# Kernel optimization log

Hardware: AMD Instinct MI355X
Metric: run time of the kernel (lower is better)

Reference implementation:

```python
import jax, jax.numpy as jnp
import numpy as np

ALPHA = 0.5  # self.alpha


def gcn_conv(x, ei, W, b, n_nodes):
    """PyG GCNConv: sym-normalized A+I aggregation of x @ W.T, plus bias."""
    h = x @ W.T  # [N, H]
    sl = jnp.arange(n_nodes)
    row = jnp.concatenate([ei[0], sl])  # sources (+ self loops)
    col = jnp.concatenate([ei[1], sl])  # targets (+ self loops)
    deg = jax.ops.segment_sum(jnp.ones_like(row, dtype=h.dtype), col, num_segments=n_nodes)
    dinv = jnp.where(deg > 0, jax.lax.rsqrt(deg), 0.0)
    norm = dinv[row] * dinv[col]
    msg = norm[:, None] * h[row]
    out = jax.ops.segment_sum(msg, col, num_segments=n_nodes)
    return out + b


def attention(Ws, A, bA):
    """Bilinear cross-view attention over weight matrices Ws [V, K, D].
    attn[i,j] = sum_k (Ws[i,k] @ A @ Ws[j,k] + bias); row-softmax."""
    K = Ws.shape[1]
    T = jnp.einsum('vka,ab->vkb', Ws, A)
    M = jnp.einsum('vkb,wkb->vw', T, Ws) + K * bA[0]
    return jax.nn.softmax(M, axis=1)


def cross_rep(x_inner, x_lin, att, alpha):
    # temp_i = alpha * sum_j att[i,j] * x_lin[j]; res = (1-alpha) + x_inner + elu(temp)
    cross = alpha * jnp.einsum('vw,wnh->vnh', att, x_lin)
    return (1.0 - alpha) + x_inner + jax.nn.elu(cross)


def setup_inputs() -> dict:
    key = jax.random.key(0)
    ks = jax.random.split(key, 20)
    N, D, H, V, E, Eev = 50000, 128, 128, 3, 800000, 100000
    s_d = 1.0 / np.sqrt(D)
    s_h = 1.0 / np.sqrt(H)
    s_c = 1.0 / np.sqrt(V * H)
    inp = {
        'x': jax.random.normal(ks[0], (N, D), dtype=jnp.float32),
        'W1': jax.random.normal(ks[1], (V, H, D), dtype=jnp.float32) * s_d,
        'b1': jnp.zeros((V, H), dtype=jnp.float32),
        'W2': jax.random.normal(ks[2], (V, H, H), dtype=jnp.float32) * s_h,
        'b2': jnp.zeros((V, H), dtype=jnp.float32),
        'A1': jax.random.normal(ks[3], (D, D), dtype=jnp.float32) * s_d,
        'bA1': jnp.zeros((1,), dtype=jnp.float32),
        'A2': jax.random.normal(ks[4], (H, H), dtype=jnp.float32) * s_h,
        'bA2': jnp.zeros((1,), dtype=jnp.float32),
        'Wc1': jax.random.normal(ks[5], (H, V * H), dtype=jnp.float32) * s_c,
        'bc1': jnp.zeros((H,), dtype=jnp.float32),
        'Wc2': jax.random.normal(ks[6], (H, V * H), dtype=jnp.float32) * s_c,
        'bc2': jnp.zeros((H,), dtype=jnp.float32),
        'edge_index': jax.random.randint(ks[7], (V, 2, E), 0, N, dtype=jnp.int64),
        'edges': jax.random.randint(ks[8], (V, Eev, 2), 0, N, dtype=jnp.int64),
        'edges_neg': jax.random.randint(ks[9], (V, Eev, 2), 0, N, dtype=jnp.int64),
    }
    return inp


def reference(x, W1, b1, W2, b2, A1, bA1, A2, bA2, Wc1, bc1, Wc2, bc2,
              edge_index, edges, edges_neg):
    N = x.shape[0]
    V = W1.shape[0]

    # layer 1: per-view GCNConv + ELU (dropout = identity in eval)
    x1 = jnp.stack([jax.nn.elu(gcn_conv(x, edge_index[v], W1[v], b1[v], N))
                    for v in range(V)])  # [V, N, H]
    xlin1 = jnp.einsum('nd,vhd->vnh', x, W1)  # conv.lin(x) per view
    att1 = attention(W1, A1, bA1)
    xr1 = cross_rep(x1, xlin1, att1, ALPHA)

    # combine 1: concat views along feature dim, linear + ELU
    emb = xr1.transpose(1, 0, 2).reshape(N, -1)  # [N, V*H]
    xc = jax.nn.elu(emb @ Wc1.T + bc1)  # [N, H]

    # layer 2: per-view GCNConv (no activation before cross rep)
    x2 = jnp.stack([gcn_conv(xc, edge_index[v], W2[v], b2[v], N)
                    for v in range(V)])
    xlin2 = jnp.einsum('nd,vhd->vnh', xc, W2)
    att2 = attention(W2, A2, bA2)
    xr2 = cross_rep(x2, xlin2, att2, ALPHA)

    # per-view edge scoring: dot products on pos then neg edges, concatenated
    def score(xv, e_pos, e_neg):
        p = jnp.sum(xv[e_pos[:, 0]] * xv[e_pos[:, 1]], axis=-1)
        n = jnp.sum(xv[e_neg[:, 0]] * xv[e_neg[:, 1]], axis=-1)
        return jnp.concatenate([p, n])

    results = jax.vmap(score)(xr2, edges, edges_neg)  # [V, 2*Eev]
    return results
```

## Files before the change

kernel.cpp:

```cpp
#include <hip/hip_runtime.h>
#include <hip/hip_bf16.h>


#define THREADS 256
#define BCH 8192

typedef __bf16 bf16x8 __attribute__((ext_vector_type(8)));
typedef float f32x4 __attribute__((ext_vector_type(4)));
typedef unsigned short us8 __attribute__((ext_vector_type(8)));

__device__ __forceinline__ float eluf(float x) {
    return x > 0.f ? x : expm1f(x);
}

__device__ __forceinline__ unsigned short f2bf(float f) {
    unsigned u = __builtin_bit_cast(unsigned, f);
    u += 0x7FFF + ((u >> 16) & 1);
    return (unsigned short)(u >> 16);
}
__device__ __forceinline__ float bf2f(unsigned short s) {
    unsigned u = ((unsigned)s) << 16;
    return __builtin_bit_cast(float, u);
}

__global__ __launch_bounds__(THREADS) void init_int_kernel(int* p, int n) {
    int i = blockIdx.x * THREADS + threadIdx.x;
    if (i < n) p[i] = 0;
}


__global__ __launch_bounds__(THREADS) void bucket_count_kernel(
    const int* __restrict__ ei, int* __restrict__ bcnt, int N, int E, int VE) {
    __shared__ int h[160];
    for (int i = threadIdx.x; i < 160; i += THREADS) h[i] = 0;
    __syncthreads();
    int base = blockIdx.x * BCH;
    for (int k = 0; k < BCH; k += THREADS) {
        int t = base + k + threadIdx.x;
        if (t < VE) {
            int v = (t >= E) + (t >= 2 * E);
            int e = t - v * E;
            int col = ei[(size_t)v * 2 * E + E + e];
            atomicAdd(&h[(v * N + col) >> 10], 1);
        }
    }
    __syncthreads();
    for (int i = threadIdx.x; i < 160; i += THREADS)
        if (h[i]) atomicAdd(&bcnt[i], h[i]);
}

__global__ __launch_bounds__(THREADS) void bucket_scan_kernel(
    const int* __restrict__ bcnt, int* __restrict__ bstart, int* __restrict__ bofs, int nb) {
    __shared__ int sh[THREADS];
    int t = threadIdx.x;
    int v = (t < nb) ? bcnt[t] : 0;
    sh[t] = v;
    __syncthreads();
    for (int off = 1; off < THREADS; off <<= 1) {
        int u = (t >= off) ? sh[t - off] : 0;
        __syncthreads();
        sh[t] += u;
        __syncthreads();
    }
    int excl = sh[t] - v;
    if (t < nb) { bstart[t] = excl; bofs[t] = excl; }
    if (t == nb - 1) bstart[nb] = sh[t];
}

__global__ __launch_bounds__(THREADS) void bucket_scatter_kernel(
    const int* __restrict__ ei, int* __restrict__ bofs,
    int* __restrict__ coo_g, int* __restrict__ coo_r, int N, int E, int VE) {
    __shared__ int h[160];
    __shared__ int cur[160];
    for (int i = threadIdx.x; i < 160; i += THREADS) h[i] = 0;
    __syncthreads();
    int base = blockIdx.x * BCH;
    for (int k = 0; k < BCH; k += THREADS) {
        int t = base + k + threadIdx.x;
        if (t < VE) {
            int v = (t >= E) + (t >= 2 * E);
            int e = t - v * E;
            int col = ei[(size_t)v * 2 * E + E + e];
            atomicAdd(&h[(v * N + col) >> 10], 1);
        }
    }
    __syncthreads();
    if (threadIdx.x < 160 && h[threadIdx.x])
        cur[threadIdx.x] = atomicAdd(&bofs[threadIdx.x], h[threadIdx.x]);
    __syncthreads();
    for (int k = 0; k < BCH; k += THREADS) {
        int t = base + k + threadIdx.x;
        if (t < VE) {
            int v = (t >= E) + (t >= 2 * E);
            int e = t - v * E;
            const int* eiv = ei + (size_t)v * 2 * E;
            int row = eiv[e], col = eiv[E + e];
            int g = v * N + col;
            int pos = atomicAdd(&cur[g >> 10], 1);
            coo_g[pos] = g;
            coo_r[pos] = row;
        }
    }
}

__global__ __launch_bounds__(THREADS) void bucket_hist_kernel(
    const int* __restrict__ coo_g, const int* __restrict__ bstart,
    int* __restrict__ cnt, int VN) {
    __shared__ int h[1024];
    for (int i = threadIdx.x; i < 1024; i += THREADS) h[i] = 0;
    __syncthreads();
    int b = blockIdx.x;
    int s = bstart[b], e = bstart[b + 1];
    for (int i = s + threadIdx.x; i < e; i += THREADS)
        atomicAdd(&h[coo_g[i] & 1023], 1);
    __syncthreads();
    int g0 = b << 10;
    for (int i = threadIdx.x; i < 1024; i += THREADS)
        if (g0 + i < VN) cnt[g0 + i] = h[i];
}

__global__ __launch_bounds__(THREADS) void bucket_fill_kernel(
    const int* __restrict__ coo_g, const int* __restrict__ coo_r,
    const int* __restrict__ bstart, int* __restrict__ ptr,
    int* __restrict__ idx, int VN) {
    __shared__ int p[1024];
    int b = blockIdx.x, g0 = b << 10;
    for (int i = threadIdx.x; i < 1024; i += THREADS)
        p[i] = (g0 + i < VN) ? ptr[g0 + i] : 0;
    __syncthreads();
    int s = bstart[b], e = bstart[b + 1];
    for (int i = s + threadIdx.x; i < e; i += THREADS) {
        int pos = atomicAdd(&p[coo_g[i] & 1023], 1);
        idx[pos] = coo_r[i];
    }
    __syncthreads();
    for (int i = threadIdx.x; i < 1024; i += THREADS)
        if (g0 + i < VN) ptr[g0 + i] = p[i];
}

#define SC_T 256
#define SC_CHUNK 1024

__global__ __launch_bounds__(SC_T) void scan_sum_kernel(
    const int* __restrict__ cnt, int* __restrict__ bsum, int n) {
    __shared__ int red[SC_T];
    int base = blockIdx.x * SC_CHUNK + threadIdx.x * 4;
    int s = 0;
#pragma unroll
    for (int k = 0; k < 4; k++) {
        int i = base + k;
        if (i < n) s += cnt[i];
    }
    red[threadIdx.x] = s;
    __syncthreads();
    for (int st = SC_T / 2; st; st >>= 1) {
        if (threadIdx.x < st) red[threadIdx.x] += red[threadIdx.x + st];
        __syncthreads();
    }
    if (threadIdx.x == 0) bsum[blockIdx.x] = red[0];
}

__global__ __launch_bounds__(SC_T) void scan_top_kernel(int* bsum, int nb) {
    __shared__ int sh[SC_T];
    int t = threadIdx.x;
    int v = (t < nb) ? bsum[t] : 0;
    sh[t] = v;
    __syncthreads();
    for (int off = 1; off < SC_T; off <<= 1) {
        int u = (t >= off) ? sh[t - off] : 0;
        __syncthreads();
        sh[t] += u;
        __syncthreads();
    }
    if (t < nb) bsum[t] = sh[t] - v;
}

__global__ __launch_bounds__(SC_T) void scan_apply_kernel(
    const int* __restrict__ cnt, const int* __restrict__ bsum,
    int* __restrict__ ptr, float* __restrict__ dinv, int n) {
    __shared__ int sh[SC_T];
    int base = blockIdx.x * SC_CHUNK + threadIdx.x * 4;
    int v[4];
    int s = 0;
#pragma unroll
    for (int k = 0; k < 4; k++) {
        int i = base + k;
        v[k] = (i < n) ? cnt[i] : 0;
        s += v[k];
    }
    int tin = s;
    sh[threadIdx.x] = s;
    __syncthreads();
    for (int off = 1; off < SC_T; off <<= 1) {
        int u = (threadIdx.x >= off) ? sh[threadIdx.x - off] : 0;
        __syncthreads();
        sh[threadIdx.x] += u;
        __syncthreads();
    }
    int run = bsum[blockIdx.x] + sh[threadIdx.x] - tin;
#pragma unroll
    for (int k = 0; k < 4; k++) {
        int i = base + k;
        if (i < n) {
            ptr[i] = run;
            run += v[k];
            dinv[i] = rsqrtf((float)(v[k] + 1));
        }
    }
}

template <int ABF>
__global__ __launch_bounds__(256) void gemm_bf16_kernel(
    const float* __restrict__ Af, const unsigned short* __restrict__ Ab,
    const float* __restrict__ B, const float* __restrict__ bias,
    unsigned short* __restrict__ C, const float* __restrict__ dscale,
    int M, int Kb, size_t AV, size_t Bz, size_t Cz) {
    __shared__ unsigned short Ah[128 * 64];
    __shared__ unsigned short Bh[128 * 64];
    int tid = threadIdx.x;
    int z = blockIdx.z;
    int m0 = blockIdx.x * 128;
    const float* Bp = B + (size_t)z * Bz;
    int lane = tid & 63, wid = tid >> 6;
    int wr = wid >> 1, wc = wid & 1;
    int lr = lane & 15, lg = lane >> 4;
    f32x4 acc[4][4] = {};

    for (int k0 = 0; k0 < Kb; k0 += 64) {
        size_t Abase = (size_t)(k0 >> 7) * AV + (k0 & 127);
        for (int i = 0; i < 4; ++i) {
            int ch = tid + i * 256;
            int row = ch >> 3, c8 = (ch & 7) << 3;
            int e = (row * 64 + c8) ^ ((row & 7) << 3);
            int gm = m0 + row;
            us8 h8;
            if (ABF) {
                if (gm < M) {
                    h8 = *(const us8*)(Ab + Abase + (size_t)gm * 128 + c8);
                } else {
#pragma unroll
                    for (int j = 0; j < 8; j++) h8[j] = 0;
                }
            } else {
                float va[8];
                if (gm < M) {
                    const float* p = Af + Abase + (size_t)gm * 128 + c8;
                    *(float4*)(va)     = *(const float4*)(p);
                    *(float4*)(va + 4) = *(const float4*)(p + 4);
                } else {
#pragma unroll
                    for (int j = 0; j < 8; j++) va[j] = 0.f;
                }
#pragma unroll
                for (int j = 0; j < 8; j++) h8[j] = f2bf(va[j]);
            }
            *(us8*)&Ah[e] = h8;
            float vb[8];
            const float* q = Bp + (size_t)row * Kb + k0 + c8;
            *(float4*)(vb)     = *(const float4*)(q);
            *(float4*)(vb + 4) = *(const float4*)(q + 4);
            us8 b8;
#pragma unroll
            for (int j = 0; j < 8; j++) b8[j] = f2bf(vb[j]);
            *(us8*)&Bh[e] = b8;
        }
        __syncthreads();
#pragma unroll
        for (int ks = 0; ks < 2; ++ks) {
            bf16x8 ah[4], bh[4];
#pragma unroll
            for (int m = 0; m < 4; m++) {
                int row = wr * 64 + m * 16 + lr;
                int e = (row * 64 + ks * 32 + lg * 8) ^ ((row & 7) << 3);
                ah[m] = *(const bf16x8*)&Ah[e];
            }
#pragma unroll
            for (int n = 0; n < 4; n++) {
                int col = wc * 64 + n * 16 + lr;
                int e = (col * 64 + ks * 32 + lg * 8) ^ ((col & 7) << 3);
                bh[n] = *(const bf16x8*)&Bh[e];
            }
#pragma unroll
            for (int m = 0; m < 4; m++)
#pragma unroll
                for (int n = 0; n < 4; n++)
                    acc[m][n] = __builtin_amdgcn_mfma_f32_16x16x32_bf16(ah[m], bh[n], acc[m][n], 0, 0, 0);
        }
        __syncthreads();
    }

#pragma unroll
    for (int m = 0; m < 4; m++) {
        int rbase = m0 + wr * 64 + m * 16 + lg * 4;
#pragma unroll
        for (int n = 0; n < 4; n++) {
            int col = wc * 64 + n * 16 + lr;
#pragma unroll
            for (int j = 0; j < 4; j++) {
                int row = rbase + j;
                if (row < M) {
                    float vv = acc[m][n][j];
                    if (bias) vv = eluf(vv + bias[col]);
                    if (dscale) vv *= dscale[(size_t)z * M + row];
                    C[(size_t)z * Cz + (size_t)row * 128 + col] = f2bf(vv);
                }
            }
        }
    }
}

__global__ __launch_bounds__(THREADS) void small_mm_nn_kernel(
    const float* __restrict__ W1, const float* __restrict__ W2,
    const float* __restrict__ A1, const float* __restrict__ A2,
    float* __restrict__ T) {
    int lin = blockIdx.x * THREADS + threadIdx.x;
    if (lin >= 2 * 3 * 128 * 128) return;
    int l = lin / 49152;
    int rem = lin - l * 49152;
    int b = rem & 127;
    int vk = rem >> 7;
    const float* w = (l ? W2 : W1) + (size_t)vk * 128;
    const float* A = l ? A2 : A1;
    float s = 0.f;
#pragma unroll 8
    for (int a = 0; a < 128; a++) s += w[a] * A[a * 128 + b];
    T[lin] = s;
}

__global__ __launch_bounds__(THREADS) void att_reduce_kernel(
    const float* __restrict__ T, const float* __restrict__ W1,
    const float* __restrict__ W2, const float* __restrict__ bA1,
    const float* __restrict__ bA2, float* __restrict__ Mraw) {
    int l = blockIdx.x / 9;
    int vw = blockIdx.x - l * 9;
    int v = vw / 3, w = vw - v * 3;
    const float* tp = T + (size_t)l * 49152 + (size_t)v * 16384;
    const float* wp = (l ? W2 : W1) + (size_t)w * 16384;
    float s = 0.f;
    for (int i = threadIdx.x; i < 16384; i += THREADS) s += tp[i] * wp[i];
    __shared__ float red[THREADS];
    red[threadIdx.x] = s;
    __syncthreads();
    for (int st = THREADS / 2; st; st >>= 1) {
        if (threadIdx.x < st) red[threadIdx.x] += red[threadIdx.x + st];
        __syncthreads();
    }
    if (threadIdx.x == 0) Mraw[blockIdx.x] = red[0] + 128.f * (l ? bA2[0] : bA1[0]);
}

__global__ void att_softmax_kernel(const float* __restrict__ Mraw, float* __restrict__ att) {
    int v = threadIdx.x;
    if (v >= 6) return;
    float m0 = Mraw[v * 3 + 0], m1 = Mraw[v * 3 + 1], m2 = Mraw[v * 3 + 2];
    float mx = fmaxf(m0, fmaxf(m1, m2));
    float e0 = expf(m0 - mx), e1 = expf(m1 - mx), e2 = expf(m2 - mx);
    float s = e0 + e1 + e2;
    att[v * 3 + 0] = e0 / s;
    att[v * 3 + 1] = e1 / s;
    att[v * 3 + 2] = e2 / s;
}

__global__ __launch_bounds__(THREADS) void gather_cross_kernel(
    const unsigned short* __restrict__ xs, const float* __restrict__ dinv,
    const int* __restrict__ ptr, const int* __restrict__ idx,
    const float* __restrict__ att, const float* __restrict__ bias,
    unsigned short* __restrict__ xr, int N, int elu_inner) {
    int wv = (blockIdx.x * THREADS + threadIdx.x) >> 6;
    int lane = threadIdx.x & 63;
    int VN = 3 * N;
    if (wv >= VN) return;
    int v = wv / N;
    int n = wv - v * N;
    int vN = v * N;
    int g = lane >> 4, f0 = (lane & 15) * 8;

    float acc[8] = {};
    int s = (wv == 0) ? 0 : ptr[wv - 1];
    int e = ptr[wv];
    int j = s + g;
    for (; j + 12 < e; j += 16) {
        int r0 = idx[j], r1 = idx[j + 4], r2 = idx[j + 8], r3 = idx[j + 12];
        us8 u0 = *(const us8*)(xs + (((size_t)(vN + r0)) << 7) + f0);
        us8 u1 = *(const us8*)(xs + (((size_t)(vN + r1)) << 7) + f0);
        us8 u2 = *(const us8*)(xs + (((size_t)(vN + r2)) << 7) + f0);
        us8 u3 = *(const us8*)(xs + (((size_t)(vN + r3)) << 7) + f0);
#pragma unroll
        for (int i = 0; i < 8; i++)
            acc[i] += (bf2f(u0[i]) + bf2f(u1[i])) + (bf2f(u2[i]) + bf2f(u3[i]));
    }
    for (; j < e; j += 4) {
        int r0 = idx[j];
        us8 u0 = *(const us8*)(xs + (((size_t)(vN + r0)) << 7) + f0);
#pragma unroll
        for (int i = 0; i < 8; i++) acc[i] += bf2f(u0[i]);
    }
#pragma unroll
    for (int i = 0; i < 8; i++) {
        acc[i] += __shfl_xor(acc[i], 16);
        acc[i] += __shfl_xor(acc[i], 32);
    }

    if (g == 0) {
        us8 su = *(const us8*)(xs + (((size_t)wv) << 7) + f0);
        float dc = dinv[wv];
        size_t nb = (((size_t)n) << 7) + f0;
        size_t NH = ((size_t)N) << 7;
        us8 c0 = *(const us8*)(xs + nb);
        us8 c1 = *(const us8*)(xs + NH + nb);
        us8 c2 = *(const us8*)(xs + 2 * NH + nb);
        float wa = att[v * 3 + 0] / dinv[n];
        float wb = att[v * 3 + 1] / dinv[N + n];
        float wc = att[v * 3 + 2] / dinv[2 * N + n];
        float4 bb0 = *(const float4*)(bias + v * 128 + f0);
        float4 bb1 = *(const float4*)(bias + v * 128 + f0 + 4);
        float bv[8] = {bb0.x, bb0.y, bb0.z, bb0.w, bb1.x, bb1.y, bb1.z, bb1.w};
        us8 o;
#pragma unroll
        for (int i = 0; i < 8; i++) {
            float a = dc * (acc[i] + bf2f(su[i])) + bv[i];
            if (elu_inner) a = eluf(a);
            float cr = wa * bf2f(c0[i]) + wb * bf2f(c1[i]) + wc * bf2f(c2[i]);
            o[i] = f2bf(0.5f + a + eluf(0.5f * cr));
        }
        *(us8*)(xr + (((size_t)wv) << 7) + f0) = o;
    }
}

__global__ __launch_bounds__(THREADS) void edge_score_kernel(
    const unsigned short* __restrict__ xr2, const int* __restrict__ edges,
    const int* __restrict__ edges_neg, float* __restrict__ out, int N, int Eev, int V) {
    int q = (blockIdx.x * THREADS + threadIdx.x) >> 4;
    int l16 = threadIdx.x & 15;
    int total = V * 2 * Eev;
    if (q >= total) return;
    int v = q / (2 * Eev);
    int r = q - v * (2 * Eev);
    const int* ep = (r < Eev) ? edges + ((size_t)v * Eev + r) * 2
                              : edges_neg + ((size_t)v * Eev + (r - Eev)) * 2;
    int a = ep[0], b = ep[1];
    const unsigned short* pa = xr2 + (((size_t)v * N + a) << 7) + l16 * 8;
    const unsigned short* pb = xr2 + (((size_t)v * N + b) << 7) + l16 * 8;
    us8 ua = *(const us8*)pa, ub = *(const us8*)pb;
    float s = 0.f;
#pragma unroll
    for (int i = 0; i < 8; i++) s += bf2f(ua[i]) * bf2f(ub[i]);
    s += __shfl_xor(s, 8);
    s += __shfl_xor(s, 4);
    s += __shfl_xor(s, 2);
    s += __shfl_xor(s, 1);
    if (l16 == 0) out[q] = s;
}

extern "C" void kernel_launch(void* const* d_in, const int* in_sizes, int n_in,
                              void* d_out, int out_size, void* d_ws, size_t ws_size,
                              hipStream_t stream) {
    const float* x   = (const float*)d_in[0];
    const float* W1  = (const float*)d_in[1];
    const float* b1  = (const float*)d_in[2];
    const float* W2  = (const float*)d_in[3];
    const float* b2  = (const float*)d_in[4];
    const float* A1  = (const float*)d_in[5];
    const float* bA1 = (const float*)d_in[6];
    const float* A2  = (const float*)d_in[7];
    const float* bA2 = (const float*)d_in[8];
    const float* Wc1 = (const float*)d_in[9];
    const float* bc1 = (const float*)d_in[10];
    const int* ei        = (const int*)d_in[13];
    const int* edges     = (const int*)d_in[14];
    const int* edges_neg = (const int*)d_in[15];
    float* out = (float*)d_out;

    const int H = 128, V = 3;
    const int N = in_sizes[0] / H;
    const int E = in_sizes[13] / (V * 2);
    const int Eev = in_sizes[14] / (V * 2);
    const int VNH = V * N * H;
    const int VN = V * N;
    const int VE = V * E;
    const int NB = (VN + 1023) >> 10;

    float* ws   = (float*)d_ws;
    float* dinv = ws;
    float* T    = dinv + VN;
    float* Mraw = T + 98304;
    float* att  = Mraw + 32;
    int* cnt    = (int*)(att + 32);
    int* ptr    = cnt + VN;
    int* bsum   = ptr + VN;
    int* bcnt   = bsum + 256;
    int* bstart = bcnt + 256;
    int* bofs   = bstart + 256;
    int* idx    = bofs + 256;
    int* coo_g  = idx + VE;
    int* coo_r  = coo_g + VE;
    unsigned short* xs = (unsigned short*)(coo_r + VE);
    unsigned short* xr = xs + VNH;
    unsigned short* xc = xr + VNH;
    (void)ws_size; (void)n_in; (void)out_size;

    dim3 blk(THREADS);
    int gBC = (VE + BCH - 1) / BCH;
    int gGather = (int)(((size_t)VN * 64 + THREADS - 1) / THREADS);
    int nScanB = (VN + SC_CHUNK - 1) / SC_CHUNK;
    dim3 gemmGrid((N + 127) / 128, 1, V);
    dim3 gemmGrid1((N + 127) / 128, 1, 1);
    int gScore = (int)(((size_t)V * 2 * Eev * 16 + THREADS - 1) / THREADS);

    init_int_kernel<<<1, blk, 0, stream>>>(bcnt, 256);
    bucket_count_kernel<<<gBC, blk, 0, stream>>>(ei, bcnt, N, E, VE);
    bucket_scan_kernel<<<1, blk, 0, stream>>>(bcnt, bstart, bofs, NB);
    bucket_scatter_kernel<<<gBC, blk, 0, stream>>>(ei, bofs, coo_g, coo_r, N, E, VE);
    bucket_hist_kernel<<<NB, blk, 0, stream>>>(coo_g, bstart, cnt, VN);
    scan_sum_kernel<<<nScanB, SC_T, 0, stream>>>(cnt, bsum, VN);
    scan_top_kernel<<<1, SC_T, 0, stream>>>(bsum, nScanB);
    scan_apply_kernel<<<nScanB, SC_T, 0, stream>>>(cnt, bsum, ptr, dinv, VN);
    bucket_fill_kernel<<<NB, blk, 0, stream>>>(coo_g, coo_r, bstart, ptr, idx, VN);

    small_mm_nn_kernel<<<(2 * 49152 + THREADS - 1) / THREADS, blk, 0, stream>>>(W1, W2, A1, A2, T);
    att_reduce_kernel<<<18, blk, 0, stream>>>(T, W1, W2, bA1, bA2, Mraw);
    att_softmax_kernel<<<1, 64, 0, stream>>>(Mraw, att);

    gemm_bf16_kernel<0><<<gemmGrid, blk, 0, stream>>>(
        x, nullptr, W1, nullptr, xs, dinv, N, 128, (size_t)0, (size_t)128 * 128, (size_t)N * 128);
    gather_cross_kernel<<<gGather, blk, 0, stream>>>(xs, dinv, ptr, idx, att, b1, xr, N, 1);

    gemm_bf16_kernel<1><<<gemmGrid1, blk, 0, stream>>>(
        nullptr, xr, Wc1, bc1, xc, nullptr, N, 384, (size_t)N * 128, (size_t)0, (size_t)0);

    gemm_bf16_kernel<1><<<gemmGrid, blk, 0, stream>>>(
        nullptr, xc, W2, nullptr, xs, dinv, N, 128, (size_t)0, (size_t)128 * 128, (size_t)N * 128);
    gather_cross_kernel<<<gGather, blk, 0, stream>>>(xs, dinv, ptr, idx, att + 9, b2, xr, N, 0);

    edge_score_kernel<<<gScore, blk, 0, stream>>>(xr, edges, edges_neg, out, N, Eev, V);
}
```

Before: 584.7 us.

## Fuse CSR hist/scan/fill into one per-bucket kernel and pre-convert x to bf16

Replaces the global histogram, three-kernel scan and fill with a single per-bucket kernel. It builds the local histogram, does a block scan offset by the bucket start, writes ptr and dinv, and scatters indices. This removes four launches and the cnt/bsum global round trips. It also adds a pass that converts x to bf16 once, so the first GEMM reads bf16 for all three views instead of converting fp32 per view. The conversion costs an extra read/write pass over x and a new workspace buffer.

```diff
diff --git a/kernel.cpp b/kernel.cpp
--- a/kernel.cpp
+++ b/kernel.cpp
@@ -26,6 +26,20 @@
 __global__ __launch_bounds__(THREADS) void init_int_kernel(int* p, int n) {
     int i = blockIdx.x * THREADS + threadIdx.x;
     if (i < n) p[i] = 0;
+}
+
+__global__ __launch_bounds__(THREADS) void f32_to_bf16_kernel(
+    const float* __restrict__ in, unsigned short* __restrict__ out, int n8) {
+    int i = blockIdx.x * THREADS + threadIdx.x;
+    if (i >= n8) return;
+    const float* p = in + (size_t)i * 8;
+    float va[8];
+    *(float4*)(va)     = *(const float4*)(p);
+    *(float4*)(va + 4) = *(const float4*)(p + 4);
+    us8 o;
+#pragma unroll
+    for (int j = 0; j < 8; j++) o[j] = f2bf(va[j]);
+    *(us8*)(out + (size_t)i * 8) = o;
 }
 
 
@@ -103,109 +117,48 @@
     }
 }
 
-__global__ __launch_bounds__(THREADS) void bucket_hist_kernel(
-    const int* __restrict__ coo_g, const int* __restrict__ bstart,
-    int* __restrict__ cnt, int VN) {
-    __shared__ int h[1024];
-    for (int i = threadIdx.x; i < 1024; i += THREADS) h[i] = 0;
-    __syncthreads();
-    int b = blockIdx.x;
-    int s = bstart[b], e = bstart[b + 1];
-    for (int i = s + threadIdx.x; i < e; i += THREADS)
-        atomicAdd(&h[coo_g[i] & 1023], 1);
-    __syncthreads();
-    int g0 = b << 10;
-    for (int i = threadIdx.x; i < 1024; i += THREADS)
-        if (g0 + i < VN) cnt[g0 + i] = h[i];
-}
-
-__global__ __launch_bounds__(THREADS) void bucket_fill_kernel(
+__global__ __launch_bounds__(THREADS) void bucket_csr_kernel(
     const int* __restrict__ coo_g, const int* __restrict__ coo_r,
     const int* __restrict__ bstart, int* __restrict__ ptr,
-    int* __restrict__ idx, int VN) {
-    __shared__ int p[1024];
+    float* __restrict__ dinv, int* __restrict__ idx, int VN) {
+    __shared__ int h[1024];
+    __shared__ int cur[1024];
+    __shared__ int sh[THREADS];
     int b = blockIdx.x, g0 = b << 10;
-    for (int i = threadIdx.x; i < 1024; i += THREADS)
-        p[i] = (g0 + i < VN) ? ptr[g0 + i] : 0;
+    int t = threadIdx.x;
+    for (int i = t; i < 1024; i += THREADS) h[i] = 0;
     __syncthreads();
     int s = bstart[b], e = bstart[b + 1];
-    for (int i = s + threadIdx.x; i < e; i += THREADS) {
-        int pos = atomicAdd(&p[coo_g[i] & 1023], 1);
+    for (int i = s + t; i < e; i += THREADS)
+        atomicAdd(&h[coo_g[i] & 1023], 1);
+    __syncthreads();
+    int v0 = h[4 * t], v1 = h[4 * t + 1], v2 = h[4 * t + 2], v3 = h[4 * t + 3];
+    int tsum = v0 + v1 + v2 + v3;
+    sh[t] = tsum;
+    __syncthreads();
+    for (int off = 1; off < THREADS; off <<= 1) {
+        int u = (t >= off) ? sh[t - off] : 0;
+        __syncthreads();
+        sh[t] += u;
+        __syncthreads();
+    }
+    int run = s + sh[t] - tsum;
+    int starts[4] = {run, run + v0, run + v0 + v1, run + v0 + v1 + v2};
+    int vals[4] = {v0, v1, v2, v3};
+#pragma unroll
+    for (int k = 0; k < 4; k++) {
+        int li = 4 * t + k;
+        cur[li] = starts[k];
+        int g = g0 + li;
+        if (g < VN) {
+            ptr[g] = starts[k] + vals[k];
+            dinv[g] = rsqrtf((float)(vals[k] + 1));
+        }
+    }
+    __syncthreads();
+    for (int i = s + t; i < e; i += THREADS) {
+        int pos = atomicAdd(&cur[coo_g[i] & 1023], 1);
         idx[pos] = coo_r[i];
-    }
-    __syncthreads();
-    for (int i = threadIdx.x; i < 1024; i += THREADS)
-        if (g0 + i < VN) ptr[g0 + i] = p[i];
-}
-
-#define SC_T 256
-#define SC_CHUNK 1024
-
-__global__ __launch_bounds__(SC_T) void scan_sum_kernel(
-    const int* __restrict__ cnt, int* __restrict__ bsum, int n) {
-    __shared__ int red[SC_T];
-    int base = blockIdx.x * SC_CHUNK + threadIdx.x * 4;
-    int s = 0;
-#pragma unroll
-    for (int k = 0; k < 4; k++) {
-        int i = base + k;
-        if (i < n) s += cnt[i];
-    }
-    red[threadIdx.x] = s;
-    __syncthreads();
-    for (int st = SC_T / 2; st; st >>= 1) {
-        if (threadIdx.x < st) red[threadIdx.x] += red[threadIdx.x + st];
-        __syncthreads();
-    }
-    if (threadIdx.x == 0) bsum[blockIdx.x] = red[0];
-}
-
-__global__ __launch_bounds__(SC_T) void scan_top_kernel(int* bsum, int nb) {
-    __shared__ int sh[SC_T];
-    int t = threadIdx.x;
-    int v = (t < nb) ? bsum[t] : 0;
-    sh[t] = v;
-    __syncthreads();
-    for (int off = 1; off < SC_T; off <<= 1) {
-        int u = (t >= off) ? sh[t - off] : 0;
-        __syncthreads();
-        sh[t] += u;
-        __syncthreads();
-    }
-    if (t < nb) bsum[t] = sh[t] - v;
-}
-
-__global__ __launch_bounds__(SC_T) void scan_apply_kernel(
-    const int* __restrict__ cnt, const int* __restrict__ bsum,
-    int* __restrict__ ptr, float* __restrict__ dinv, int n) {
-    __shared__ int sh[SC_T];
-    int base = blockIdx.x * SC_CHUNK + threadIdx.x * 4;
-    int v[4];
-    int s = 0;
-#pragma unroll
-    for (int k = 0; k < 4; k++) {
-        int i = base + k;
-        v[k] = (i < n) ? cnt[i] : 0;
-        s += v[k];
-    }
-    int tin = s;
-    sh[threadIdx.x] = s;
-    __syncthreads();
-    for (int off = 1; off < SC_T; off <<= 1) {
-        int u = (threadIdx.x >= off) ? sh[threadIdx.x - off] : 0;
-        __syncthreads();
-        sh[threadIdx.x] += u;
-        __syncthreads();
-    }
-    int run = bsum[blockIdx.x] + sh[threadIdx.x] - tin;
-#pragma unroll
-    for (int k = 0; k < 4; k++) {
-        int i = base + k;
-        if (i < n) {
-            ptr[i] = run;
-            run += v[k];
-            dinv[i] = rsqrtf((float)(v[k] + 1));
-        }
     }
 }
 
@@ -484,10 +437,8 @@
     float* T    = dinv + VN;
     float* Mraw = T + 98304;
     float* att  = Mraw + 32;
-    int* cnt    = (int*)(att + 32);
-    int* ptr    = cnt + VN;
-    int* bsum   = ptr + VN;
-    int* bcnt   = bsum + 256;
+    int* ptr    = (int*)(att + 32);
+    int* bcnt   = ptr + VN;
     int* bstart = bcnt + 256;
     int* bofs   = bstart + 256;
     int* idx    = bofs + 256;
@@ -496,32 +447,31 @@
     unsigned short* xs = (unsigned short*)(coo_r + VE);
     unsigned short* xr = xs + VNH;
     unsigned short* xc = xr + VNH;
+    unsigned short* xb = xc + (size_t)N * H;
     (void)ws_size; (void)n_in; (void)out_size;
 
     dim3 blk(THREADS);
     int gBC = (VE + BCH - 1) / BCH;
     int gGather = (int)(((size_t)VN * 64 + THREADS - 1) / THREADS);
-    int nScanB = (VN + SC_CHUNK - 1) / SC_CHUNK;
     dim3 gemmGrid((N + 127) / 128, 1, V);
     dim3 gemmGrid1((N + 127) / 128, 1, 1);
     int gScore = (int)(((size_t)V * 2 * Eev * 16 + THREADS - 1) / THREADS);
+    int n8 = N * H / 8;
 
     init_int_kernel<<<1, blk, 0, stream>>>(bcnt, 256);
     bucket_count_kernel<<<gBC, blk, 0, stream>>>(ei, bcnt, N, E, VE);
     bucket_scan_kernel<<<1, blk, 0, stream>>>(bcnt, bstart, bofs, NB);
     bucket_scatter_kernel<<<gBC, blk, 0, stream>>>(ei, bofs, coo_g, coo_r, N, E, VE);
-    bucket_hist_kernel<<<NB, blk, 0, stream>>>(coo_g, bstart, cnt, VN);
-    scan_sum_kernel<<<nScanB, SC_T, 0, stream>>>(cnt, bsum, VN);
-    scan_top_kernel<<<1, SC_T, 0, stream>>>(bsum, nScanB);
-    scan_apply_kernel<<<nScanB, SC_T, 0, stream>>>(cnt, bsum, ptr, dinv, VN);
-    bucket_fill_kernel<<<NB, blk, 0, stream>>>(coo_g, coo_r, bstart, ptr, idx, VN);
+    bucket_csr_kernel<<<NB, blk, 0, stream>>>(coo_g, coo_r, bstart, ptr, dinv, idx, VN);
+
+    f32_to_bf16_kernel<<<(n8 + THREADS - 1) / THREADS, blk, 0, stream>>>(x, xb, n8);
 
     small_mm_nn_kernel<<<(2 * 49152 + THREADS - 1) / THREADS, blk, 0, stream>>>(W1, W2, A1, A2, T);
     att_reduce_kernel<<<18, blk, 0, stream>>>(T, W1, W2, bA1, bA2, Mraw);
     att_softmax_kernel<<<1, 64, 0, stream>>>(Mraw, att);
 
-    gemm_bf16_kernel<0><<<gemmGrid, blk, 0, stream>>>(
-        x, nullptr, W1, nullptr, xs, dinv, N, 128, (size_t)0, (size_t)128 * 128, (size_t)N * 128);
+    gemm_bf16_kernel<1><<<gemmGrid, blk, 0, stream>>>(
+        nullptr, xb, W1, nullptr, xs, dinv, N, 128, (size_t)0, (size_t)128 * 128, (size_t)N * 128);
     gather_cross_kernel<<<gGather, blk, 0, stream>>>(xs, dinv, ptr, idx, att, b1, xr, N, 1);
 
     gemm_bf16_kernel<1><<<gemmGrid1, blk, 0, stream>>>(
```

Result: faster. 544.7 us (-6.8%).
